# Kernel optimization log

Measured on AMD Instinct MI355X. Metric: run time of the kernel, lower is better.

Reference implementation:

```python
import jax, jax.numpy as jnp
import numpy as np

T, B, N = 512, 256, 128


def setup_inputs() -> dict:
    key = jax.random.key(0)
    k1, k2, k3, k4, k5, k6 = jax.random.split(key, 6)
    emit = jax.random.normal(k1, (T, B, N), dtype=jnp.float32)
    target = jax.random.randint(k2, (T, B), 0, N, dtype=jnp.int32)
    # monotone mask: each sequence has length in [T//2, T]
    lengths = jax.random.randint(k3, (B,), T // 2, T + 1, dtype=jnp.int32)
    mask = jnp.arange(T, dtype=jnp.int32)[:, None] < lengths[None, :]
    trans = 0.1 * jax.random.normal(k4, (N, N), dtype=jnp.float32)
    strans = 0.1 * jax.random.normal(k5, (N,), dtype=jnp.float32)
    etrans = 0.1 * jax.random.normal(k6, (N,), dtype=jnp.float32)
    return {"emit": emit, "target": target, "mask": mask,
            "trans": trans, "strans": strans, "etrans": etrans}


def _crf_nll(emit, trans, strans, etrans, target, mask):
    t_len, b, n = emit.shape

    # ---- logZ: forward algorithm (sequential scan over time) ----
    def step(alpha, inp):
        emit_i, mask_i = inp  # [B,N], [B]
        # scores[b, j, k] = alpha[b, j] + trans[j, k] + emit_i[b, k]
        scores = jax.nn.logsumexp(
            alpha[:, :, None] + trans[None, :, :] + emit_i[:, None, :], axis=1)
        alpha = jnp.where(mask_i[:, None], scores, alpha)
        return alpha, None

    alpha0 = strans[None, :] + emit[0]  # [B,N]
    alpha, _ = jax.lax.scan(step, alpha0, (emit[1:], mask[1:]))
    logZ = jax.nn.logsumexp(alpha + etrans[None, :], axis=1).sum()

    # ---- gold score ----
    emit_sc = jnp.take_along_axis(emit, target[:, :, None], axis=2)[..., 0]  # [T,B]
    trans_sc = trans[target[:-1], target[1:]]  # [T-1,B]
    scores = emit_sc.at[1:].add(trans_sc)
    score = jnp.where(mask, scores, 0.0).sum()
    ends = mask.sum(axis=0) - 1  # [B]
    score = score + strans[target[0]].sum()
    score = score + etrans[target[ends, jnp.arange(b)]].sum()

    return (logZ - score) / b


def reference(emit, target, mask, trans, strans, etrans):
    return _crf_nll(emit, trans, strans, etrans, target, mask)
```

## Files before the change

### kernel.cpp

```cpp
#include <hip/hip_runtime.h>

#define T_LEN 512
#define B_SZ  256
#define N_ST  128

#if defined(__has_builtin)
# if __has_builtin(__builtin_amdgcn_fdot2_f32_bf16)
#  define HAVE_DOT2 1
# endif
#endif
#ifndef HAVE_DOT2
# define HAVE_DOT2 0
#endif

typedef unsigned int uint32;
typedef __bf16 bf16x2 __attribute__((ext_vector_type(2)));

__device__ __forceinline__ uint32 bf16rn(float f) {
    uint32 u = __builtin_bit_cast(uint32, f);
    u += 0x7fffu + ((u >> 16) & 1u);
    return u >> 16;
}
__device__ __forceinline__ uint32 pack2(float lo, float hi) {
    return bf16rn(lo) | (bf16rn(hi) << 16);
}
__device__ __forceinline__ uint32 cvtpk(float lo, float hi) {
    uint32 r;
    asm("v_cvt_pk_bf16_f32 %0, %1, %2" : "=v"(r) : "v"(lo), "v"(hi));
    return r;
}
__device__ __forceinline__ float readlane0(float v) {
    return __builtin_bit_cast(float, (uint32)__builtin_amdgcn_readlane(__builtin_bit_cast(int, v), 0));
}
__device__ __forceinline__ float dot2b(uint32 a, uint32 b, float c) {
#if HAVE_DOT2
    return __builtin_amdgcn_fdot2_f32_bf16(__builtin_bit_cast(bf16x2, a),
                                           __builtin_bit_cast(bf16x2, b), c, false);
#else
    float alo = __builtin_bit_cast(float, a << 16);
    float ahi = __builtin_bit_cast(float, a & 0xffff0000u);
    float blo = __builtin_bit_cast(float, b << 16);
    float bhi = __builtin_bit_cast(float, b & 0xffff0000u);
    return fmaf(ahi, bhi, fmaf(alo, blo, c));
#endif
}


__global__ __launch_bounds__(64) void lengths_kernel(const unsigned char* __restrict__ mask_raw,
                                                     int* __restrict__ lens) {
    int b = blockIdx.x;
    int l = threadIdx.x;
    unsigned char b1 = mask_raw[1], b2 = mask_raw[2];
    int mode = (b1 != 0) ? 0 : ((b2 != 0) ? 2 : 1);
    int cnt = 0;
    if (mode == 0) {
        #pragma unroll
        for (int k = 0; k < 8; ++k) cnt += (mask_raw[(l * 8 + k) * B_SZ + b] != 0);
    } else if (mode == 1) {
        const int* m = (const int*)mask_raw;
        #pragma unroll
        for (int k = 0; k < 8; ++k) cnt += (m[(l * 8 + k) * B_SZ + b] != 0);
    } else {
        const float* m = (const float*)mask_raw;
        #pragma unroll
        for (int k = 0; k < 8; ++k) cnt += (m[(l * 8 + k) * B_SZ + b] != 0.0f);
    }
    #pragma unroll
    for (int off = 1; off < 64; off <<= 1) cnt += __shfl_xor(cnt, off);
    if (l == 0) lens[b] = cnt;
}

__global__ __launch_bounds__(128, 1) void forward_kernel(
        const float* __restrict__ emit,
        const float* __restrict__ trans,
        const float* __restrict__ strans,
        const float* __restrict__ etrans,
        const int* __restrict__ lens,
        float* __restrict__ logZ_out) {
    const int b   = blockIdx.x;
    const int tid = threadIdx.x;
    const int wid = tid >> 6;
    const int l   = tid & 63;
    const int c0  = 2 * l, c1 = 2 * l + 1;

    __shared__ alignas(16) uint32 a32[64];
    __shared__ alignas(16) uint32 z32[64];
    __shared__ float meetA[N_ST], meetY[N_ST];
    __shared__ float maccSh[2], red2[2];

    const int len = lens[b];
    const int m = (len - 1 < 256) ? (len - 1) : 256;
    const float* eb = emit + (size_t)b * N_ST;
    const size_t TS = (size_t)B_SZ * N_ST;

    if (wid == 0) {
        uint32 EA[64], EB[64];
        #pragma unroll
        for (int p = 0; p < 64; ++p) {
            EA[p] = pack2(__expf(trans[(2 * p) * N_ST + c0]), __expf(trans[(2 * p + 1) * N_ST + c0]));
            EB[p] = pack2(__expf(trans[(2 * p) * N_ST + c1]), __expf(trans[(2 * p + 1) * N_ST + c1]));
        }
        float aA = __expf(strans[c0] + eb[c0]);
        float aB = __expf(strans[c1] + eb[c1]);
        a32[l] = pack2(aA, aB);
        float Macc = 0.f, inv = 1.0f;
        float ec0 = eb[TS + c0],      ec1 = eb[TS + c1];
        float en0 = eb[2 * TS + c0],  en1 = eb[2 * TS + c1];
        for (int t = 1; t <= m; ++t) {
            const size_t t2 = (size_t)((t + 2 <= m) ? t + 2 : m) * TS;
            const float e20 = eb[t2 + c0], e21 = eb[t2 + c1];
            const float ee0 = __expf(ec0), ee1 = __expf(ec1);
            float A0 = 0, A1 = 0, A2 = 0, A3 = 0, B0 = 0, B1 = 0, B2 = 0, B3 = 0;
            #pragma unroll
            for (int q = 0; q < 16; ++q) {
                uint4 w;
                __builtin_memcpy(&w, (const char*)a32 + 16 * q, 16);
                A0 = dot2b(w.x, EA[4 * q + 0], A0);  B0 = dot2b(w.x, EB[4 * q + 0], B0);
                A1 = dot2b(w.y, EA[4 * q + 1], A1);  B1 = dot2b(w.y, EB[4 * q + 1], B1);
                A2 = dot2b(w.z, EA[4 * q + 2], A2);  B2 = dot2b(w.z, EB[4 * q + 2], B2);
                A3 = dot2b(w.w, EA[4 * q + 3], A3);  B3 = dot2b(w.w, EB[4 * q + 3], B3);
            }
            const float rA = (A0 + A1) + (A2 + A3);
            const float rB = (B0 + B1) + (B2 + B3);
            Macc -= __logf(inv);
            aA = ee0 * rA * inv;
            aB = ee1 * rB * inv;
            a32[l] = cvtpk(aA, aB);
            inv = __builtin_amdgcn_rcpf(readlane0(rA));
            ec0 = en0; ec1 = en1; en0 = e20; en1 = e21;
        }
        meetA[c0] = aA; meetA[c1] = aB;
        if (l == 0) maccSh[0] = Macc;
    } else {
        uint32 RA[64], RB[64];
        #pragma unroll
        for (int p = 0; p < 64; ++p) {
            RA[p] = pack2(__expf(trans[c0 * N_ST + 2 * p]), __expf(trans[c0 * N_ST + 2 * p + 1]));
            RB[p] = pack2(__expf(trans[c1 * N_ST + 2 * p]), __expf(trans[c1 * N_ST + 2 * p + 1]));
        }
        float y0 = __expf(etrans[c0]);
        float y1 = __expf(etrans[c1]);
        float Maccb = 0.f, invb = 1.0f;
        const int t0 = len - 1;
        float ec0 = eb[(size_t)t0 * TS + c0], ec1 = eb[(size_t)t0 * TS + c1];
        float en0 = ec0, en1 = ec1;
        if (t0 - 1 > m) { en0 = eb[(size_t)(t0 - 1) * TS + c0]; en1 = eb[(size_t)(t0 - 1) * TS + c1]; }
        for (int t = t0; t > m; --t) {
            const int tp = (t - 2 > m) ? t - 2 : m + 1;
            const float e20 = eb[(size_t)tp * TS + c0], e21 = eb[(size_t)tp * TS + c1];
            const float ee0 = __expf(ec0), ee1 = __expf(ec1);
            z32[l] = cvtpk(ee0 * y0, ee1 * y1);
            float R0 = 0, R1 = 0, R2 = 0, R3 = 0, S0 = 0, S1 = 0, S2 = 0, S3 = 0;
            #pragma unroll
            for (int q = 0; q < 16; ++q) {
                uint4 w;
                __builtin_memcpy(&w, (const char*)z32 + 16 * q, 16);
                R0 = dot2b(w.x, RA[4 * q + 0], R0);  S0 = dot2b(w.x, RB[4 * q + 0], S0);
                R1 = dot2b(w.y, RA[4 * q + 1], R1);  S1 = dot2b(w.y, RB[4 * q + 1], S1);
                R2 = dot2b(w.z, RA[4 * q + 2], R2);  S2 = dot2b(w.z, RB[4 * q + 2], S2);
                R3 = dot2b(w.w, RA[4 * q + 3], R3);  S3 = dot2b(w.w, RB[4 * q + 3], S3);
            }
            const float rR = (R0 + R1) + (R2 + R3);
            const float rS = (S0 + S1) + (S2 + S3);
            Maccb -= __logf(invb);
            y0 = rR * invb;
            y1 = rS * invb;
            invb = __builtin_amdgcn_rcpf(readlane0(rR));
            ec0 = en0; ec1 = en1; en0 = e20; en1 = e21;
        }
        meetY[c0] = y0; meetY[c1] = y1;
        if (l == 0) maccSh[1] = Maccb;
    }

    __syncthreads();
    float v = meetA[tid] * meetY[tid];
    #pragma unroll
    for (int off = 1; off < 64; off <<= 1) v += __shfl_xor(v, off);
    if (l == 0) red2[wid] = v;
    __syncthreads();
    if (tid == 0) logZ_out[b] = maccSh[0] + maccSh[1] + __logf(red2[0] + red2[1]);
}

__global__ __launch_bounds__(128) void score_kernel(
        const float* __restrict__ emit,
        const int* __restrict__ target,
        const float* __restrict__ trans,
        const float* __restrict__ strans,
        const float* __restrict__ etrans,
        const int* __restrict__ lens,
        float* __restrict__ score_out) {
    const int b   = blockIdx.x;
    const int tid = threadIdx.x;
    const int len = lens[b];
    float local = 0.f;
    for (int t = tid; t < len; t += 128) {
        int tgt = target[t * B_SZ + b];
        float v = emit[(size_t)t * (B_SZ * N_ST) + b * N_ST + tgt];
        if (t > 0) v += trans[target[(t - 1) * B_SZ + b] * N_ST + tgt];
        local += v;
    }
    if (tid == 0) {
        local += strans[target[b]];
        local += etrans[target[(len - 1) * B_SZ + b]];
    }
    #pragma unroll
    for (int off = 1; off < 64; off <<= 1) local += __shfl_xor(local, off);
    __shared__ float partial[2];
    if ((tid & 63) == 0) partial[tid >> 6] = local;
    __syncthreads();
    if (tid == 0) score_out[b] = partial[0] + partial[1];
}

__global__ __launch_bounds__(256) void finalize_kernel(
        const float* __restrict__ logZ,
        const float* __restrict__ score,
        float* __restrict__ out) {
    int tid = threadIdx.x;
    float v = logZ[tid] - score[tid];
    #pragma unroll
    for (int off = 1; off < 64; off <<= 1) v += __shfl_xor(v, off);
    __shared__ float p[4];
    if ((tid & 63) == 0) p[tid >> 6] = v;
    __syncthreads();
    if (tid == 0) out[0] = (p[0] + p[1] + p[2] + p[3]) / 256.0f;
}

extern "C" void kernel_launch(void* const* d_in, const int* in_sizes, int n_in,
                              void* d_out, int out_size, void* d_ws, size_t ws_size,
                              hipStream_t stream) {
    const float*         emit   = (const float*)d_in[0];
    const int*           target = (const int*)d_in[1];
    const unsigned char* mask   = (const unsigned char*)d_in[2];
    const float*         trans  = (const float*)d_in[3];
    const float*         strans = (const float*)d_in[4];
    const float*         etrans = (const float*)d_in[5];

    float* ws     = (float*)d_ws;
    float* logZb  = ws;
    float* scoreb = ws + 256;
    int*   lens   = (int*)(ws + 512);

    lengths_kernel<<<B_SZ, 64, 0, stream>>>(mask, lens);
    forward_kernel<<<B_SZ, 128, 0, stream>>>(emit, trans, strans, etrans, lens, logZb);
    score_kernel<<<B_SZ, 128, 0, stream>>>(emit, target, trans, strans, etrans, lens, scoreb);
    finalize_kernel<<<1, 256, 0, stream>>>(logZb, scoreb, (float*)d_out);
}
```

Before: 125.9 us.

## Batch 16 sequences per block and run CRF recurrence on MFMA bf16 matrix cores

Replaces the per-sequence forward/backward dot2 kernel with a batched kernel where each block handles 16 sequences and computes the exp-domain transition matmul with 16x16x32 bf16 MFMA instructions. Forward blocks and backward blocks run in parallel and meet in the middle, writing partial states to workspace, and a new combine kernel reduces them into logZ. The aim is to cut per-step latency and raise the work done per step by using the matrix cores. In exchange it adds a block-wide barrier every step, iterates to the maximum length within each 16-sequence group, and needs an extra launch plus workspace. It keeps the old kernel as a fallback when the workspace is too small.

```diff
diff --git a/kernel.cpp b/kernel.cpp
--- a/kernel.cpp
+++ b/kernel.cpp
@@ -13,26 +13,25 @@
 # define HAVE_DOT2 0
 #endif
 
-typedef unsigned int uint32;
+typedef unsigned int u32;
+typedef short s8v __attribute__((ext_vector_type(8)));
+typedef float f4v __attribute__((ext_vector_type(4)));
 typedef __bf16 bf16x2 __attribute__((ext_vector_type(2)));
 
-__device__ __forceinline__ uint32 bf16rn(float f) {
-    uint32 u = __builtin_bit_cast(uint32, f);
+__device__ __forceinline__ u32 bf16rn(float f) {
+    u32 u = __builtin_bit_cast(u32, f);
     u += 0x7fffu + ((u >> 16) & 1u);
     return u >> 16;
 }
-__device__ __forceinline__ uint32 pack2(float lo, float hi) {
+__device__ __forceinline__ u32 pack2(float lo, float hi) {
     return bf16rn(lo) | (bf16rn(hi) << 16);
 }
-__device__ __forceinline__ uint32 cvtpk(float lo, float hi) {
-    uint32 r;
+__device__ __forceinline__ u32 cvtpk(float lo, float hi) {
+    u32 r;
     asm("v_cvt_pk_bf16_f32 %0, %1, %2" : "=v"(r) : "v"(lo), "v"(hi));
     return r;
 }
-__device__ __forceinline__ float readlane0(float v) {
-    return __builtin_bit_cast(float, (uint32)__builtin_amdgcn_readlane(__builtin_bit_cast(int, v), 0));
-}
-__device__ __forceinline__ float dot2b(uint32 a, uint32 b, float c) {
+__device__ __forceinline__ float dot2b(u32 a, u32 b, float c) {
 #if HAVE_DOT2
     return __builtin_amdgcn_fdot2_f32_bf16(__builtin_bit_cast(bf16x2, a),
                                            __builtin_bit_cast(bf16x2, b), c, false);
@@ -44,7 +43,39 @@
     return fmaf(ahi, bhi, fmaf(alo, blo, c));
 #endif
 }
-
+__device__ __forceinline__ float readlane0(float v) {
+    return __builtin_bit_cast(float, (u32)__builtin_amdgcn_readlane(__builtin_bit_cast(int, v), 0));
+}
+
+
+template <bool TR>
+__device__ __forceinline__ s8v loadAE(const float* __restrict__ trans, int mt, int ks, int n, int g) {
+    const int m = 16 * mt + n;
+    uint4 q;
+    #define LA(I, DST) { const int e0 = 2*(I), e1 = 2*(I)+1; \
+        const int k0 = 16*(2*ks + (e0 >> 2)) + 4*g + (e0 & 3); \
+        const int k1 = 16*(2*ks + (e1 >> 2)) + 4*g + (e1 & 3); \
+        const float f0 = TR ? trans[k0 * N_ST + m] : trans[m * N_ST + k0]; \
+        const float f1 = TR ? trans[k1 * N_ST + m] : trans[m * N_ST + k1]; \
+        DST = cvtpk(__expf(f0), __expf(f1)); }
+    LA(0, q.x) LA(1, q.y) LA(2, q.z) LA(3, q.w)
+    #undef LA
+    return __builtin_bit_cast(s8v, q);
+}
+
+__device__ __forceinline__ uint4 initBv(const float* __restrict__ row,
+                                        const float* __restrict__ bias, int g, int ks) {
+    uint4 q;
+    #define IB(I, DST) { const int e0 = 2*(I), e1 = 2*(I)+1; \
+        const int m0 = 16*(2*ks + (e0 >> 2)) + 4*g + (e0 & 3); \
+        const int m1 = 16*(2*ks + (e1 >> 2)) + 4*g + (e1 & 3); \
+        DST = cvtpk(__expf(bias[m0] + row[m0]), __expf(bias[m1] + row[m1])); }
+    IB(0, q.x) IB(1, q.y) IB(2, q.z) IB(3, q.w)
+    #undef IB
+    return q;
+}
+
+#define WS_NEED_BYTES (34048 * 4)
 
 __global__ __launch_bounds__(64) void lengths_kernel(const unsigned char* __restrict__ mask_raw,
                                                      int* __restrict__ lens) {
@@ -70,31 +101,218 @@
     if (l == 0) lens[b] = cnt;
 }
 
-__global__ __launch_bounds__(128, 1) void forward_kernel(
+#define MCHAIN(DST, A0_, A1_, A2_, A3_) { \
+    const f4v z_ = {0.f, 0.f, 0.f, 0.f}; \
+    DST = __builtin_amdgcn_mfma_f32_16x16x32_bf16(A0_, B0, z_, 0, 0, 0); \
+    DST = __builtin_amdgcn_mfma_f32_16x16x32_bf16(A1_, B1, DST, 0, 0, 0); \
+    DST = __builtin_amdgcn_mfma_f32_16x16x32_bf16(A2_, B2, DST, 0, 0, 0); \
+    DST = __builtin_amdgcn_mfma_f32_16x16x32_bf16(A3_, B3, DST, 0, 0, 0); }
+
+__global__ __launch_bounds__(256, 1) void fb_kernel(
         const float* __restrict__ emit,
         const float* __restrict__ trans,
         const float* __restrict__ strans,
         const float* __restrict__ etrans,
         const int* __restrict__ lens,
-        float* __restrict__ logZ_out) {
-    const int b   = blockIdx.x;
+        float* __restrict__ wsMF, float* __restrict__ wsMB,
+        uint4* __restrict__ wsU, uint4* __restrict__ wsZ) {
+    const int isF = (blockIdx.x < 16);
+    const int tl  = isF ? blockIdx.x : (blockIdx.x - 16);
+    const int tid = threadIdx.x;
+    const int w = tid >> 6, l = tid & 63, g = l >> 4, n = l & 15;
+    const int bn = tl * 16 + n;
+
+    __shared__ uint4 xch[2][4][64];
+    __shared__ float dsh[2][16];
+
+    const size_t TS = (size_t)B_SZ * N_ST;
+    const int len_n = lens[bn];
+    const int m_n = (len_n - 2 < 255) ? (len_n - 2) : 255;
+    const float* eeb = emit + (size_t)bn * N_ST + 32 * w + 4 * g;
+
+    s8v B0, B1, B2, B3;
+    uint4 my;
+    float Macc = 0.f, sclog = 0.f, inv = 1.0f;
+    int pp = 0;
+    f4v LBa, LBb, LCa, LCb, EEa, EEb;
+
+    if (isF) {
+        const s8v Aa0 = loadAE<true>(trans, 2 * w,     0, n, g);
+        const s8v Aa1 = loadAE<true>(trans, 2 * w,     1, n, g);
+        const s8v Aa2 = loadAE<true>(trans, 2 * w,     2, n, g);
+        const s8v Aa3 = loadAE<true>(trans, 2 * w,     3, n, g);
+        const s8v Ab0 = loadAE<true>(trans, 2 * w + 1, 0, n, g);
+        const s8v Ab1 = loadAE<true>(trans, 2 * w + 1, 1, n, g);
+        const s8v Ab2 = loadAE<true>(trans, 2 * w + 1, 2, n, g);
+        const s8v Ab3 = loadAE<true>(trans, 2 * w + 1, 3, n, g);
+
+        int tmax = m_n;
+        #pragma unroll
+        for (int off = 1; off < 16; off <<= 1) tmax = max(tmax, __shfl_xor(tmax, off));
+
+        const float* e0 = emit + (size_t)bn * N_ST;
+        const uint4 b0 = initBv(e0, strans, g, 0);
+        const uint4 b1 = initBv(e0, strans, g, 1);
+        const uint4 b2 = initBv(e0, strans, g, 2);
+        const uint4 b3 = initBv(e0, strans, g, 3);
+        B0 = __builtin_bit_cast(s8v, b0);  B1 = __builtin_bit_cast(s8v, b1);
+        B2 = __builtin_bit_cast(s8v, b2);  B3 = __builtin_bit_cast(s8v, b3);
+        my = (w == 0) ? b0 : (w == 1) ? b1 : (w == 2) ? b2 : b3;
+
+        LBa = *(const f4v*)(eeb + TS);       LBb = *(const f4v*)(eeb + 16 + TS);
+        EEa = f4v{__expf(LBa.x), __expf(LBa.y), __expf(LBa.z), __expf(LBa.w)};
+        EEb = f4v{__expf(LBb.x), __expf(LBb.y), __expf(LBb.z), __expf(LBb.w)};
+        {
+            const size_t t2 = (size_t)((2 <= tmax) ? 2 : tmax) * TS;
+            LBa = *(const f4v*)(eeb + t2);   LBb = *(const f4v*)(eeb + 16 + t2);
+        }
+
+        for (int t = 1; t <= tmax; ++t) {
+            const size_t tp = (size_t)((t + 2 <= tmax) ? t + 2 : tmax) * TS;
+            LCa = *(const f4v*)(eeb + tp);   LCb = *(const f4v*)(eeb + 16 + tp);
+            const bool cond = (t <= m_n);
+            Macc += cond ? sclog : 0.0f;
+            f4v Da, Db;
+            MCHAIN(Da, Aa0, Aa1, Aa2, Aa3)
+            MCHAIN(Db, Ab0, Ab1, Ab2, Ab3)
+            if (w == 0 && l < 16) dsh[pp][l] = Da.x;
+            const f4v sa = Da * EEa, sb = Db * EEb;
+            uint4 nw;
+            nw.x = cvtpk(sa.x, sa.y);  nw.y = cvtpk(sa.z, sa.w);
+            nw.z = cvtpk(sb.x, sb.y);  nw.w = cvtpk(sb.z, sb.w);
+            my.x = cond ? nw.x : my.x;  my.y = cond ? nw.y : my.y;
+            my.z = cond ? nw.z : my.z;  my.w = cond ? nw.w : my.w;
+            xch[pp][w][l] = my;
+            __syncthreads();
+            B0 = __builtin_bit_cast(s8v, xch[pp][0][l]);
+            B1 = __builtin_bit_cast(s8v, xch[pp][1][l]);
+            B2 = __builtin_bit_cast(s8v, xch[pp][2][l]);
+            B3 = __builtin_bit_cast(s8v, xch[pp][3][l]);
+            const float d00 = dsh[pp][n];
+            inv = __builtin_amdgcn_rcpf(d00);
+            sclog = -__logf(inv);
+            EEa = f4v{__expf(LBa.x), __expf(LBa.y), __expf(LBa.z), __expf(LBa.w)} * inv;
+            EEb = f4v{__expf(LBb.x), __expf(LBb.y), __expf(LBb.z), __expf(LBb.w)} * inv;
+            LBa = LCa; LBb = LCb;
+            pp ^= 1;
+        }
+        f4v Da, Db;
+        MCHAIN(Da, Aa0, Aa1, Aa2, Aa3)
+        MCHAIN(Db, Ab0, Ab1, Ab2, Ab3)
+        uint4 uw;
+        uw.x = cvtpk(Da.x, Da.y);  uw.y = cvtpk(Da.z, Da.w);
+        uw.z = cvtpk(Db.x, Db.y);  uw.w = cvtpk(Db.z, Db.w);
+        wsU[(tl * 4 + w) * 64 + l] = uw;
+        if (w == 0 && l < 16) wsMF[tl * 16 + l] = Macc;
+    } else {
+        const s8v Aa0 = loadAE<false>(trans, 2 * w,     0, n, g);
+        const s8v Aa1 = loadAE<false>(trans, 2 * w,     1, n, g);
+        const s8v Aa2 = loadAE<false>(trans, 2 * w,     2, n, g);
+        const s8v Aa3 = loadAE<false>(trans, 2 * w,     3, n, g);
+        const s8v Ab0 = loadAE<false>(trans, 2 * w + 1, 0, n, g);
+        const s8v Ab1 = loadAE<false>(trans, 2 * w + 1, 1, n, g);
+        const s8v Ab2 = loadAE<false>(trans, 2 * w + 1, 2, n, g);
+        const s8v Ab3 = loadAE<false>(trans, 2 * w + 1, 3, n, g);
+
+        int smax = len_n - 1, smin = m_n + 1;
+        #pragma unroll
+        for (int off = 1; off < 16; off <<= 1) {
+            smax = max(smax, __shfl_xor(smax, off));
+            smin = min(smin, __shfl_xor(smin, off));
+        }
+        const uint4 Zi = initBv(emit + (size_t)(len_n - 1) * TS + (size_t)bn * N_ST, etrans, g, w);
+        const uint4 z4 = {0u, 0u, 0u, 0u};
+        B0 = __builtin_bit_cast(s8v, z4);  B1 = B0;  B2 = B0;  B3 = B0;
+        my = z4;
+
+        LBa = *(const f4v*)(eeb + (size_t)smax * TS);
+        LBb = *(const f4v*)(eeb + 16 + (size_t)smax * TS);
+        EEa = f4v{__expf(LBa.x), __expf(LBa.y), __expf(LBa.z), __expf(LBa.w)};
+        EEb = f4v{__expf(LBb.x), __expf(LBb.y), __expf(LBb.z), __expf(LBb.w)};
+        {
+            const size_t s1 = (size_t)((smax - 1 >= smin) ? smax - 1 : smin) * TS;
+            LBa = *(const f4v*)(eeb + s1);   LBb = *(const f4v*)(eeb + 16 + s1);
+        }
+
+        for (int s = smax; s >= smin; --s) {
+            const size_t sp = (size_t)((s - 2 >= smin) ? s - 2 : smin) * TS;
+            LCa = *(const f4v*)(eeb + sp);   LCb = *(const f4v*)(eeb + 16 + sp);
+            const bool condS = (s >= m_n + 1) && (s <= len_n - 2);
+            const bool condI = (s == len_n - 1);
+            Macc += condS ? sclog : 0.0f;
+            f4v Da, Db;
+            MCHAIN(Da, Aa0, Aa1, Aa2, Aa3)
+            MCHAIN(Db, Ab0, Ab1, Ab2, Ab3)
+            if (w == 0 && l < 16) dsh[pp][l] = Da.x;
+            const f4v sa = Da * EEa, sb = Db * EEb;
+            uint4 nw;
+            nw.x = cvtpk(sa.x, sa.y);  nw.y = cvtpk(sa.z, sa.w);
+            nw.z = cvtpk(sb.x, sb.y);  nw.w = cvtpk(sb.z, sb.w);
+            my.x = condI ? Zi.x : (condS ? nw.x : my.x);
+            my.y = condI ? Zi.y : (condS ? nw.y : my.y);
+            my.z = condI ? Zi.z : (condS ? nw.z : my.z);
+            my.w = condI ? Zi.w : (condS ? nw.w : my.w);
+            xch[pp][w][l] = my;
+            __syncthreads();
+            B0 = __builtin_bit_cast(s8v, xch[pp][0][l]);
+            B1 = __builtin_bit_cast(s8v, xch[pp][1][l]);
+            B2 = __builtin_bit_cast(s8v, xch[pp][2][l]);
+            B3 = __builtin_bit_cast(s8v, xch[pp][3][l]);
+            const float d00 = dsh[pp][n];
+            inv = (d00 > 0.0f) ? __builtin_amdgcn_rcpf(d00) : 1.0f;
+            sclog = -__logf(inv);
+            EEa = f4v{__expf(LBa.x), __expf(LBa.y), __expf(LBa.z), __expf(LBa.w)} * inv;
+            EEb = f4v{__expf(LBb.x), __expf(LBb.y), __expf(LBb.z), __expf(LBb.w)} * inv;
+            LBa = LCa; LBb = LCb;
+            pp ^= 1;
+        }
+        wsZ[(tl * 4 + w) * 64 + l] = my;
+        if (w == 0 && l < 16) wsMB[tl * 16 + l] = Macc;
+    }
+}
+
+__global__ __launch_bounds__(256) void combine_kernel(
+        const uint4* __restrict__ wsU, const uint4* __restrict__ wsZ,
+        const float* __restrict__ wsMF, const float* __restrict__ wsMB,
+        float* __restrict__ logZ) {
+    const int tl = blockIdx.x;
+    const int tid = threadIdx.x;
+    const int w = tid >> 6, l = tid & 63, n = l & 15;
+    const uint4 u = wsU[(tl * 4 + w) * 64 + l];
+    const uint4 z = wsZ[(tl * 4 + w) * 64 + l];
+    float v = 0.f;
+    v = dot2b(u.x, z.x, v);  v = dot2b(u.y, z.y, v);
+    v = dot2b(u.z, z.z, v);  v = dot2b(u.w, z.w, v);
+    __shared__ float red[16][17];
+    red[n][w * 4 + (l >> 4)] = v;
+    __syncthreads();
+    if (tid < 16) {
+        float s = 0.f;
+        #pragma unroll
+        for (int i = 0; i < 16; ++i) s += red[tid][i];
+        logZ[tl * 16 + tid] = wsMF[tl * 16 + tid] + wsMB[tl * 16 + tid] + __logf(s);
+    }
+}
+
+__global__ __launch_bounds__(128, 1) void forward_fallback(
+        const float* __restrict__ emit, const float* __restrict__ trans,
+        const float* __restrict__ strans, const float* __restrict__ etrans,
+        const int* __restrict__ lens, float* __restrict__ logZ_out) {
+    const int b = blockIdx.x;
     const int tid = threadIdx.x;
     const int wid = tid >> 6;
-    const int l   = tid & 63;
-    const int c0  = 2 * l, c1 = 2 * l + 1;
-
-    __shared__ alignas(16) uint32 a32[64];
-    __shared__ alignas(16) uint32 z32[64];
+    const int l = tid & 63;
+    const int c0 = 2 * l, c1 = 2 * l + 1;
+    __shared__ alignas(16) u32 a32[64];
+    __shared__ alignas(16) u32 z32[64];
     __shared__ float meetA[N_ST], meetY[N_ST];
     __shared__ float maccSh[2], red2[2];
-
     const int len = lens[b];
     const int m = (len - 1 < 256) ? (len - 1) : 256;
     const float* eb = emit + (size_t)b * N_ST;
     const size_t TS = (size_t)B_SZ * N_ST;
-
     if (wid == 0) {
-        uint32 EA[64], EB[64];
+        u32 EA[64], EB[64];
         #pragma unroll
         for (int p = 0; p < 64; ++p) {
             EA[p] = pack2(__expf(trans[(2 * p) * N_ST + c0]), __expf(trans[(2 * p + 1) * N_ST + c0]));
@@ -104,27 +322,26 @@
         float aB = __expf(strans[c1] + eb[c1]);
         a32[l] = pack2(aA, aB);
         float Macc = 0.f, inv = 1.0f;
-        float ec0 = eb[TS + c0],      ec1 = eb[TS + c1];
-        float en0 = eb[2 * TS + c0],  en1 = eb[2 * TS + c1];
+        float ec0 = eb[TS + c0], ec1 = eb[TS + c1];
+        float en0 = eb[2 * TS + c0], en1 = eb[2 * TS + c1];
         for (int t = 1; t <= m; ++t) {
             const size_t t2 = (size_t)((t + 2 <= m) ? t + 2 : m) * TS;
             const float e20 = eb[t2 + c0], e21 = eb[t2 + c1];
             const float ee0 = __expf(ec0), ee1 = __expf(ec1);
-            float A0 = 0, A1 = 0, A2 = 0, A3 = 0, B0 = 0, B1 = 0, B2 = 0, B3 = 0;
+            float A0 = 0, A1 = 0, A2 = 0, A3 = 0, Bb0 = 0, Bb1 = 0, Bb2 = 0, Bb3 = 0;
             #pragma unroll
             for (int q = 0; q < 16; ++q) {
-                uint4 w;
-                __builtin_memcpy(&w, (const char*)a32 + 16 * q, 16);
-                A0 = dot2b(w.x, EA[4 * q + 0], A0);  B0 = dot2b(w.x, EB[4 * q + 0], B0);
-                A1 = dot2b(w.y, EA[4 * q + 1], A1);  B1 = dot2b(w.y, EB[4 * q + 1], B1);
-                A2 = dot2b(w.z, EA[4 * q + 2], A2);  B2 = dot2b(w.z, EB[4 * q + 2], B2);
-                A3 = dot2b(w.w, EA[4 * q + 3], A3);  B3 = dot2b(w.w, EB[4 * q + 3], B3);
+                uint4 ww;
+                __builtin_memcpy(&ww, (const char*)a32 + 16 * q, 16);
+                A0 = dot2b(ww.x, EA[4 * q + 0], A0);  Bb0 = dot2b(ww.x, EB[4 * q + 0], Bb0);
+                A1 = dot2b(ww.y, EA[4 * q + 1], A1);  Bb1 = dot2b(ww.y, EB[4 * q + 1], Bb1);
+                A2 = dot2b(ww.z, EA[4 * q + 2], A2);  Bb2 = dot2b(ww.z, EB[4 * q + 2], Bb2);
+                A3 = dot2b(ww.w, EA[4 * q + 3], A3);  Bb3 = dot2b(ww.w, EB[4 * q + 3], Bb3);
             }
             const float rA = (A0 + A1) + (A2 + A3);
-            const float rB = (B0 + B1) + (B2 + B3);
+            const float rB = (Bb0 + Bb1) + (Bb2 + Bb3);
             Macc -= __logf(inv);
-            aA = ee0 * rA * inv;
-            aB = ee1 * rB * inv;
+            aA = ee0 * rA * inv;  aB = ee1 * rB * inv;
             a32[l] = cvtpk(aA, aB);
             inv = __builtin_amdgcn_rcpf(readlane0(rA));
             ec0 = en0; ec1 = en1; en0 = e20; en1 = e21;
@@ -132,7 +349,7 @@
         meetA[c0] = aA; meetA[c1] = aB;
         if (l == 0) maccSh[0] = Macc;
     } else {
-        uint32 RA[64], RB[64];
+        u32 RA[64], RB[64];
         #pragma unroll
         for (int p = 0; p < 64; ++p) {
             RA[p] = pack2(__expf(trans[c0 * N_ST + 2 * p]), __expf(trans[c0 * N_ST + 2 * p + 1]));
@@ -153,25 +370,23 @@
             float R0 = 0, R1 = 0, R2 = 0, R3 = 0, S0 = 0, S1 = 0, S2 = 0, S3 = 0;
             #pragma unroll
             for (int q = 0; q < 16; ++q) {
-                uint4 w;
-                __builtin_memcpy(&w, (const char*)z32 + 16 * q, 16);
-                R0 = dot2b(w.x, RA[4 * q + 0], R0);  S0 = dot2b(w.x, RB[4 * q + 0], S0);
-                R1 = dot2b(w.y, RA[4 * q + 1], R1);  S1 = dot2b(w.y, RB[4 * q + 1], S1);
-                R2 = dot2b(w.z, RA[4 * q + 2], R2);  S2 = dot2b(w.z, RB[4 * q + 2], S2);
-                R3 = dot2b(w.w, RA[4 * q + 3], R3);  S3 = dot2b(w.w, RB[4 * q + 3], S3);
+                uint4 ww;
+                __builtin_memcpy(&ww, (const char*)z32 + 16 * q, 16);
+                R0 = dot2b(ww.x, RA[4 * q + 0], R0);  S0 = dot2b(ww.x, RB[4 * q + 0], S0);
+                R1 = dot2b(ww.y, RA[4 * q + 1], R1);  S1 = dot2b(ww.y, RB[4 * q + 1], S1);
+                R2 = dot2b(ww.z, RA[4 * q + 2], R2);  S2 = dot2b(ww.z, RB[4 * q + 2], S2);
+                R3 = dot2b(ww.w, RA[4 * q + 3], R3);  S3 = dot2b(ww.w, RB[4 * q + 3], S3);
             }
             const float rR = (R0 + R1) + (R2 + R3);
             const float rS = (S0 + S1) + (S2 + S3);
             Maccb -= __logf(invb);
-            y0 = rR * invb;
-            y1 = rS * invb;
+            y0 = rR * invb;  y1 = rS * invb;
             invb = __builtin_amdgcn_rcpf(readlane0(rR));
             ec0 = en0; ec1 = en1; en0 = e20; en1 = e21;
         }
         meetY[c0] = y0; meetY[c1] = y1;
         if (l == 0) maccSh[1] = Maccb;
     }
-
     __syncthreads();
     float v = meetA[tid] * meetY[tid];
     #pragma unroll
@@ -189,7 +404,7 @@
         const float* __restrict__ etrans,
         const int* __restrict__ lens,
         float* __restrict__ score_out) {
-    const int b   = blockIdx.x;
+    const int b = blockIdx.x;
     const int tid = threadIdx.x;
     const int len = lens[b];
     float local = 0.f;
@@ -239,9 +454,18 @@
     float* logZb  = ws;
     float* scoreb = ws + 256;
     int*   lens   = (int*)(ws + 512);
+    float* wsMF   = ws + 768;
+    float* wsMB   = ws + 1024;
+    uint4* wsU    = (uint4*)(ws + 1280);
+    uint4* wsZ    = (uint4*)(ws + 17664);
 
     lengths_kernel<<<B_SZ, 64, 0, stream>>>(mask, lens);
-    forward_kernel<<<B_SZ, 128, 0, stream>>>(emit, trans, strans, etrans, lens, logZb);
+    if (ws_size >= (size_t)WS_NEED_BYTES) {
+        fb_kernel<<<32, 256, 0, stream>>>(emit, trans, strans, etrans, lens, wsMF, wsMB, wsU, wsZ);
+        combine_kernel<<<16, 256, 0, stream>>>(wsU, wsZ, wsMF, wsMB, logZb);
+    } else {
+        forward_fallback<<<B_SZ, 128, 0, stream>>>(emit, trans, strans, etrans, lens, logZb);
+    }
     score_kernel<<<B_SZ, 128, 0, stream>>>(emit, target, trans, strans, etrans, lens, scoreb);
     finalize_kernel<<<1, 256, 0, stream>>>(logZb, scoreb, (float*)d_out);
 }
```

Result: no change. 128.1 us (+1.8%).
